# Kernel tuning notes

Hardware: AMD Instinct MI355X
Metric: run time of the kernel (lower is better)

## Reference

```python
import jax, jax.numpy as jnp
import numpy as np
from math import sqrt

NUM_ENT = 100000
NUM_REL = 237  # base; rel table has 2*NUM_REL rows
DIM = 200
HALF = DIM // 2


def _lrelu(x, slope):
    return jnp.where(x >= 0, x, slope * x)


def setup_inputs() -> dict:
    key = jax.random.key(0)
    ks = jax.random.split(key, 20)
    s = 0.02
    inp = {
        'edge_index': jax.random.randint(ks[0], (2, 500000), 0, NUM_ENT),
        'edge_type': jax.random.randint(ks[1], (500000,), 0, 2 * NUM_REL),
        'toTest': jax.random.randint(ks[2], (131072, 2), 0, NUM_ENT),
        'ent_emb': s * jax.random.normal(ks[3], (NUM_ENT, DIM), jnp.float32),
        'rel_emb': s * jax.random.normal(ks[4], (2 * NUM_REL, DIM), jnp.float32),
        'W': s * jax.random.normal(ks[5], (DIM, DIM), jnp.float32),
        'W_loop': s * jax.random.normal(ks[6], (DIM, DIM), jnp.float32),
        'W_rel': s * jax.random.normal(ks[7], (DIM, DIM), jnp.float32),
        'trans_w': s * jax.random.normal(ks[8], (DIM, HALF), jnp.float32),
        'trans_b': jnp.zeros((HALF,), jnp.float32),
        'q_w': s * jax.random.normal(ks[9], (HALF, 128), jnp.float32),
        'q_b': jnp.zeros((128,), jnp.float32),
        'k_w': s * jax.random.normal(ks[10], (HALF, 128), jnp.float32),
        'k_b': jnp.zeros((128,), jnp.float32),
        'w1': s * jax.random.normal(ks[11], (DIM * 2 + 1 + 2 * NUM_REL, 2048), jnp.float32),
        'b1': jnp.zeros((2048,), jnp.float32),
        'w2': s * jax.random.normal(ks[12], (2048, 512), jnp.float32),
        'b2': jnp.zeros((512,), jnp.float32),
        'w3': s * jax.random.normal(ks[13], (512, 1), jnp.float32),
        'b3': jnp.zeros((1,), jnp.float32),
    }
    return inp


def reference(ent_emb, rel_emb, W, W_loop, W_rel, trans_w, trans_b,
              q_w, q_b, k_w, k_b, w1, b1, w2, b2, w3, b3,
              edge_index, edge_type, toTest):
    # --- CompGCN base layer ('sub' composition, degree-normalized scatter-add) ---
    src, dst = edge_index[0], edge_index[1]
    msg = (ent_emb[src] - rel_emb[edge_type]) @ W          # [E, D] gather + GEMM
    deg = jax.ops.segment_sum(jnp.ones_like(dst, jnp.float32), dst, num_segments=NUM_ENT)
    norm = jax.lax.rsqrt(jnp.maximum(deg, 1.0))
    agg = jax.ops.segment_sum(msg, dst, num_segments=NUM_ENT) * norm[:, None]
    all_ent = jnp.tanh(agg + ent_emb @ W_loop)             # [num_ent, D]
    all_rel = rel_emb @ W_rel                              # [2*num_rel, D]

    # --- PairRE test scoring path ---
    head_rel = all_rel[:, :HALF]                           # [2R, D/2]
    tail_rel = all_rel[:, HALF:]
    te = all_ent[toTest]                                   # [N, 2, D] gather
    ee = te @ trans_w + trans_b                            # [N, 2, D/2]
    h_e, t_e = ee[:, 0], ee[:, 1]
    atta = ((h_e @ q_w + q_b) * (t_e @ k_w + k_b)).sum(-1, keepdims=True) / sqrt(DIM)
    relSim = h_e @ head_rel.T - t_e @ tail_rel.T           # [N, 2R]
    cat = jnp.concatenate([te[:, 0], te[:, 1], atta, relSim], axis=1)
    h1 = _lrelu(cat @ w1 + b1, 1e-4)
    h2 = _lrelu(h1 @ w2 + b2, 1e-3)
    return jax.nn.sigmoid(h2 @ w3 + b3)                    # [N, 1]
```

## Files before the change

### kernel.cpp

```cpp
#include <hip/hip_runtime.h>

typedef unsigned short u16;
typedef __attribute__((ext_vector_type(8))) short bf8;
typedef __attribute__((ext_vector_type(4))) float fx4;

#define N_ENT   100000
#define N_EDGE  500000
#define N_TEST  131072
#define EDIM    200
#define AE_LD   224
#define NB_SCAN 391

__device__ __forceinline__ u16 f2bf(float f) {
  union { float f; unsigned u; } c; c.f = f;
  return (u16)((c.u + 0x7FFFu + ((c.u >> 16) & 1u)) >> 16);
}
__device__ __forceinline__ float bf2f(u16 h) {
  union { unsigned u; float f; } c; c.u = ((unsigned)h) << 16;
  return c.f;
}
__device__ __forceinline__ void gload16(const u16* g, u16* l) {
  __builtin_amdgcn_global_load_lds(
      (const __attribute__((address_space(1))) void*)g,
      (__attribute__((address_space(3))) void*)l, 16, 0, 0);
}

#define BM 128
#define BN 128
#define BK 32

__global__ __launch_bounds__(256) void gemm_bf16(
    const u16* __restrict__ A, long lda,
    const u16* __restrict__ B, long ldb,
    u16* __restrict__ out, long ldOut,
    int K,
    const int* __restrict__ rowIdx, int idxMode, int mClamp,
    int mValid, int nValid, int nStore,
    const float* __restrict__ bias, int act, float slope,
    const u16* __restrict__ qbuf, const float* __restrict__ auxF,
    float* __restrict__ dotOut)
{
  __shared__ __align__(16) u16 As[BM * BK];
  __shared__ __align__(16) u16 Bs[BN * BK];
  const int tid  = threadIdx.x;
  const int wave = tid >> 6, lane = tid & 63;
  const int wr = (wave >> 1) * 64, wc = (wave & 1) * 64;
  const int fr = lane & 15, fq = lane >> 4;
  const long bm = (long)blockIdx.x * BM, bn = (long)blockIdx.y * BN;

  const int srow = wave * 32;
  const int kc = (lane & 3) * 8;
  long a0[2], a1[2], boff[2];
  #pragma unroll
  for (int h = 0; h < 2; ++h) {
    long gmRow = bm + srow + h * 16 + (lane >> 2);
    long b0, b1;
    if (idxMode == 0) {
      long gm = (gmRow >= mClamp) ? (mClamp - 1) : gmRow;
      b0 = gm * lda; b1 = b0;
    } else if (idxMode == 2) {
      b0 = (long)rowIdx[2 * gmRow] * lda; b1 = b0;
    } else if (idxMode == 3) {
      b0 = (long)rowIdx[2 * gmRow + 1] * lda; b1 = b0;
    } else {
      b0 = (long)rowIdx[2 * gmRow] * lda;
      b1 = (long)rowIdx[2 * gmRow + 1] * lda - 224;
    }
    a0[h] = b0 + kc; a1[h] = b1 + kc;
    boff[h] = (bn + srow + h * 16 + (lane >> 2)) * ldb + kc;
  }

  fx4 zero4 = {0.f, 0.f, 0.f, 0.f};
  fx4 acc[4][4];
  #pragma unroll
  for (int i = 0; i < 4; ++i)
    #pragma unroll
    for (int j = 0; j < 4; ++j) acc[i][j] = zero4;

  for (int k0 = 0; k0 < K; k0 += BK) {
    __syncthreads();
    const bool lo = (k0 + kc) < 224;
    #pragma unroll
    for (int h = 0; h < 2; ++h) {
      const long ao = (idxMode == 4) ? (lo ? a0[h] : a1[h]) : a0[h];
      gload16(A + ao + k0, &As[(srow + h * 16) * BK]);
      gload16(B + boff[h] + k0, &Bs[(srow + h * 16) * BK]);
    }
    __syncthreads();
    bf8 aF[4], bF[4];
    #pragma unroll
    for (int mt = 0; mt < 4; ++mt) aF[mt] = *(const bf8*)&As[(wr + mt * 16 + fr) * BK + fq * 8];
    #pragma unroll
    for (int nt = 0; nt < 4; ++nt) bF[nt] = *(const bf8*)&Bs[(wc + nt * 16 + fr) * BK + fq * 8];
    #pragma unroll
    for (int mt = 0; mt < 4; ++mt)
      #pragma unroll
      for (int nt = 0; nt < 4; ++nt)
        acc[mt][nt] = __builtin_amdgcn_mfma_f32_16x16x32_bf16(aF[mt], bF[nt], acc[mt][nt], 0, 0, 0);
  }

  if (act == 3 || act == 4) {
    #pragma unroll
    for (int mt = 0; mt < 4; ++mt) {
      #pragma unroll
      for (int r = 0; r < 4; ++r) {
        const long gm = bm + wr + mt * 16 + fq * 4 + r;
        float p = 0.f;
        #pragma unroll
        for (int nt = 0; nt < 4; ++nt) {
          const long gn = bn + wc + nt * 16 + fr;
          float v = acc[mt][nt][r] + bias[gn];
          if (act == 3) p += v * bf2f(qbuf[gm * 128 + gn]);
          else { v = (v >= 0.f) ? v : v * slope; p += v * auxF[gn]; }
        }
        p += __shfl_xor(p, 1, 64); p += __shfl_xor(p, 2, 64);
        p += __shfl_xor(p, 4, 64); p += __shfl_xor(p, 8, 64);
        if (fr == 0 && gm < mValid)
          atomicAdd(&dotOut[gm], (act == 3) ? p * 0.07071067811865475f : p);
      }
    }
    return;
  }

  #pragma unroll
  for (int mt = 0; mt < 4; ++mt) {
    #pragma unroll
    for (int r = 0; r < 4; ++r) {
      const long gm = bm + wr + mt * 16 + fq * 4 + r;
      if (gm >= mValid) continue;
      const float attaV = (act == 5) ? dotOut[gm] : 0.f;
      #pragma unroll
      for (int nt = 0; nt < 4; ++nt) {
        const long gn = bn + wc + nt * 16 + fr;
        if (gn >= nStore) continue;
        float v = 0.f;
        if (gn < nValid) {
          v = acc[mt][nt][r];
          if (bias) v += bias[gn];
          if (act == 1) v = tanhf(v);
          else if (act == 5) { v += attaV * auxF[gn]; v = (v >= 0.f) ? v : v * slope; }
        }
        out[gm * ldOut + gn] = f2bf(v);
      }
    }
  }
}

__global__ void hist_kernel(const int* __restrict__ ei, int* __restrict__ cnt) {
  int e = blockIdx.x * 256 + threadIdx.x;
  if (e < N_EDGE) atomicAdd(&cnt[ei[N_EDGE + e]], 1);
}
__global__ void scanA_kernel(const int* __restrict__ cnt, int* __restrict__ offs,
                             int* __restrict__ blockSums) {
  __shared__ int s[256];
  int gid = blockIdx.x * 256 + threadIdx.x;
  int v = (gid < N_ENT) ? cnt[gid] : 0;
  s[threadIdx.x] = v;
  __syncthreads();
  for (int off = 1; off < 256; off <<= 1) {
    int t = (threadIdx.x >= off) ? s[threadIdx.x - off] : 0;
    __syncthreads();
    s[threadIdx.x] += t;
    __syncthreads();
  }
  if (gid < N_ENT) offs[gid] = s[threadIdx.x] - v;
  if (threadIdx.x == 255) blockSums[blockIdx.x] = s[255];
}
__global__ void scanB_kernel(const int* __restrict__ blockSums, int* __restrict__ blockOffs) {
  __shared__ int s[512];
  int v = (threadIdx.x < NB_SCAN) ? blockSums[threadIdx.x] : 0;
  s[threadIdx.x] = v;
  __syncthreads();
  for (int off = 1; off < 512; off <<= 1) {
    int t = (threadIdx.x >= off) ? s[threadIdx.x - off] : 0;
    __syncthreads();
    s[threadIdx.x] += t;
    __syncthreads();
  }
  if (threadIdx.x < NB_SCAN) blockOffs[threadIdx.x] = s[threadIdx.x] - v;
}
__global__ void scanC_kernel(int* __restrict__ offs, const int* __restrict__ blockOffs) {
  int gid = blockIdx.x * 256 + threadIdx.x;
  if (gid < N_ENT) offs[gid] += blockOffs[blockIdx.x];
}
__global__ void place_kernel(const int* __restrict__ ei, const int* __restrict__ et,
                             const int* __restrict__ offs, int* __restrict__ cursor,
                             int* __restrict__ sortedSrc, int* __restrict__ sortedT) {
  int e = blockIdx.x * 256 + threadIdx.x;
  if (e >= N_EDGE) return;
  int dst = ei[N_EDGE + e];
  int pos = offs[dst] + atomicAdd(&cursor[dst], 1);
  sortedSrc[pos] = ei[e];
  sortedT[pos]   = et[e];
}
__global__ void agg_A1_kernel(const int* __restrict__ offs, const int* __restrict__ cnt,
                              const int* __restrict__ sortedSrc, const int* __restrict__ sortedT,
                              const float* __restrict__ ent_emb, const float* __restrict__ rel_emb,
                              u16* __restrict__ A1) {
  const int r = blockIdx.x * 4 + (threadIdx.x >> 6);
  if (r >= N_ENT) return;
  const int lane = threadIdx.x & 63;
  const int beg = offs[r], n = cnt[r];
  float a0 = 0.f, a1 = 0.f, a2 = 0.f, a3 = 0.f;
  for (int e = 0; e < n; ++e) {
    const int s = sortedSrc[beg + e], t = sortedT[beg + e];
    const float* er = ent_emb + (size_t)s * EDIM;
    const float* rr = rel_emb + (size_t)t * EDIM;
    a0 += er[lane]       - rr[lane];
    a1 += er[64 + lane]  - rr[64 + lane];
    a2 += er[128 + lane] - rr[128 + lane];
    if (lane < 8) a3 += er[192 + lane] - rr[192 + lane];
  }
  const float nm = rsqrtf(fmaxf((float)n, 1.f));
  u16* row = A1 + (size_t)r * 416;
  row[lane]       = f2bf(a0 * nm);
  row[64 + lane]  = f2bf(a1 * nm);
  row[128 + lane] = f2bf(a2 * nm);
  if (lane < 8) row[192 + lane] = f2bf(a3 * nm);
  const float* er = ent_emb + (size_t)r * EDIM;
  row[200 + lane] = f2bf(er[lane]);
  row[264 + lane] = f2bf(er[64 + lane]);
  row[328 + lane] = f2bf(er[128 + lane]);
  if (lane < 8)  row[392 + lane] = f2bf(er[192 + lane]);
  if (lane < 16) row[400 + lane] = 0;
}

__global__ void build_B1T(const float* __restrict__ W, const float* __restrict__ W_loop,
                          u16* __restrict__ B1T)
{
  int idx = blockIdx.x * 256 + threadIdx.x;
  if (idx >= 256 * 416) return;
  int n = idx / 416, k = idx % 416;
  float v = 0.f;
  if (n < 200) {
    if (k < 200) v = W[k * 200 + n];
    else if (k < 400) v = W_loop[(k - 200) * 200 + n];
  }
  B1T[idx] = f2bf(v);
}
__global__ void all_rel_kernel(const float* __restrict__ rel_emb, const float* __restrict__ W_rel,
                               float* __restrict__ all_rel)
{
  int r = blockIdx.x, c = threadIdx.x;
  if (c >= 200) return;
  const float* re = rel_emb + r * 200;
  float a = 0.f;
  for (int k = 0; k < 200; ++k) a += re[k] * W_rel[k * 200 + c];
  all_rel[r * 200 + c] = a;
}
__global__ void pq_kernel(const float* __restrict__ all_rel, const float* __restrict__ w1,
                          float* __restrict__ PQ) {
  int idx = blockIdx.x * 256 + threadIdx.x;
  if (idx >= 2 * 100 * 2048) return;
  int n = idx & 2047, m = (idx >> 11) % 100, sel = idx / 204800;
  float a = 0.f;
  for (int r = 0; r < 474; ++r)
    a += all_rel[r * 200 + sel * 100 + m] * w1[(size_t)(401 + r) * 2048 + n];
  PQ[idx] = a;
}
__global__ void p2_kernel(const float* __restrict__ trans_w, const float* __restrict__ PQ,
                          float* __restrict__ P2) {
  int idx = blockIdx.x * 256 + threadIdx.x;
  if (idx >= 2 * 200 * 2048) return;
  int n = idx & 2047, k = (idx >> 11) % 200, sel = idx / 409600;
  const float* pq = PQ + sel * 204800;
  float a = 0.f;
  for (int m = 0; m < 100; ++m) a += trans_w[k * 100 + m] * pq[m * 2048 + n];
  P2[idx] = a;
}
__global__ void w1eff_kernel(const float* __restrict__ w1, const float* __restrict__ P2,
                             u16* __restrict__ W1eff) {
  int idx = blockIdx.x * 256 + threadIdx.x;
  if (idx >= 2048 * 448) return;
  int n = idx / 448, k = idx % 448;
  float v = 0.f;
  if (k < 200) v = w1[(size_t)k * 2048 + n] + P2[(size_t)k * 2048 + n];
  else if (k >= 224 && k < 424) {
    int kk = k - 224;
    v = w1[(size_t)(200 + kk) * 2048 + n] - P2[409600 + (size_t)kk * 2048 + n];
  }
  W1eff[idx] = f2bf(v);
}
__global__ void b1eff_kernel(const float* __restrict__ b1, const float* __restrict__ trans_b,
                             const float* __restrict__ PQ, float* __restrict__ b1eff) {
  int n = blockIdx.x * 256 + threadIdx.x;
  if (n >= 2048) return;
  float a = b1[n];
  for (int m = 0; m < 100; ++m)
    a += trans_b[m] * (PQ[m * 2048 + n] - PQ[204800 + m * 2048 + n]);
  b1eff[n] = a;
}
__global__ void qkw2_kernel(const float* __restrict__ trans_w, const float* __restrict__ q_w,
                            const float* __restrict__ k_w, u16* __restrict__ qw2T,
                            u16* __restrict__ kw2T) {
  int idx = blockIdx.x * 256 + threadIdx.x;
  if (idx >= 128 * 224) return;
  int j = idx / 224, k = idx % 224;
  float a = 0.f, b = 0.f;
  if (k < 200)
    for (int m = 0; m < 100; ++m) {
      float t = trans_w[k * 100 + m];
      a += t * q_w[m * 128 + j];
      b += t * k_w[m * 128 + j];
    }
  qw2T[idx] = f2bf(a);
  kw2T[idx] = f2bf(b);
}
__global__ void qkb2_kernel(const float* __restrict__ q_b, const float* __restrict__ k_b,
                            const float* __restrict__ trans_b, const float* __restrict__ q_w,
                            const float* __restrict__ k_w, float* __restrict__ qb2,
                            float* __restrict__ kb2) {
  int j = threadIdx.x;
  if (j >= 128) return;
  float a = q_b[j], b = k_b[j];
  for (int m = 0; m < 100; ++m) {
    a += trans_b[m] * q_w[m * 128 + j];
    b += trans_b[m] * k_w[m * 128 + j];
  }
  qb2[j] = a; kb2[j] = b;
}
__global__ void build_w2T(const float* __restrict__ w2, u16* __restrict__ w2T)
{
  long idx = (long)blockIdx.x * 256 + threadIdx.x;
  if (idx >= (long)512 * 2048) return;
  int n = (int)(idx / 2048), k = (int)(idx % 2048);
  w2T[idx] = f2bf(w2[(size_t)k * 512 + n]);
}
__global__ void sigmoid_kernel(const float* __restrict__ logit, const float* __restrict__ b3,
                               float* __restrict__ out) {
  int i = blockIdx.x * 256 + threadIdx.x;
  if (i >= N_TEST) return;
  out[i] = 1.f / (1.f + __expf(-(logit[i] + b3[0])));
}

extern "C" void kernel_launch(void* const* d_in, const int* in_sizes, int n_in,
                              void* d_out, int out_size, void* d_ws, size_t ws_size,
                              hipStream_t stream)
{
  (void)in_sizes; (void)n_in; (void)out_size;
  const int*   edge_index = (const int*)d_in[0];
  const int*   edge_type  = (const int*)d_in[1];
  const int*   toTest     = (const int*)d_in[2];
  const float* ent_emb    = (const float*)d_in[3];
  const float* rel_emb    = (const float*)d_in[4];
  const float* W          = (const float*)d_in[5];
  const float* W_loop     = (const float*)d_in[6];
  const float* W_rel      = (const float*)d_in[7];
  const float* trans_w    = (const float*)d_in[8];
  const float* trans_b    = (const float*)d_in[9];
  const float* q_w        = (const float*)d_in[10];
  const float* q_b        = (const float*)d_in[11];
  const float* k_w        = (const float*)d_in[12];
  const float* k_b        = (const float*)d_in[13];
  const float* w1         = (const float*)d_in[14];
  const float* b1         = (const float*)d_in[15];
  const float* w2         = (const float*)d_in[16];
  const float* b2         = (const float*)d_in[17];
  const float* w3         = (const float*)d_in[18];
  const float* b3         = (const float*)d_in[19];
  float* out = (float*)d_out;

  unsigned char* ws = (unsigned char*)d_ws;
  float* atta    = (float*)(ws + 0);
  float* logit   = (float*)(ws + 524288);
  float* allrel  = (float*)(ws + 1048576);
  u16*   B1T     = (u16*)  (ws + 1427968);
  u16*   W1eff   = (u16*)  (ws + 1640960);
  u16*   qw2T    = (u16*)  (ws + 3475968);
  u16*   kw2T    = (u16*)  (ws + 3533312);
  float* b1eff   = (float*)(ws + 3590656);
  float* qb2     = (float*)(ws + 3598848);
  float* kb2     = (float*)(ws + 3599872);
  u16*   w2T     = (u16*)  (ws + 3600896);
  const size_t X_base = 5698048;
  u16*   all_ent = (u16*)  (ws + X_base);
  u16*   Qbuf    = (u16*)  (ws + X_base + 44800000);
  const size_t Y_base = 84052480;
  u16*   A1      = (u16*)  (ws + Y_base);
  const size_t Z_base = 167252480;

  int*   cnt       = (int*)  (ws + Z_base);
  int*   offs      = (int*)  (ws + Z_base + 400000);
  int*   cursor    = (int*)  (ws + Z_base + 800000);
  int*   blockSums = (int*)  (ws + Z_base + 1200000);
  int*   blockOffs = (int*)  (ws + Z_base + 1202048);
  int*   sortedSrc = (int*)  (ws + Z_base + 1204096);
  int*   sortedT   = (int*)  (ws + Z_base + 3204096);
  float* PQ        = (float*)(ws + Z_base + 5204096);
  float* P2        = (float*)(ws + Z_base + 6842496);

  int CH;
  if      (Z_base + (size_t)131072 * 4096 <= ws_size) CH = 131072;
  else if (Z_base + (size_t)65536  * 4096 <= ws_size) CH = 65536;
  else if (Z_base + (size_t)32768  * 4096 <= ws_size) CH = 32768;
  else if (Z_base + (size_t)16384  * 4096 <= ws_size) CH = 16384;
  else if (Z_base + (size_t)8192   * 4096 <= ws_size) CH = 8192;
  else return;
  u16* h1 = (u16*)(ws + Z_base);
  const int NC = N_TEST / CH;

  hipMemsetAsync(cnt, 0, 400000, stream);
  hipMemsetAsync(cursor, 0, 400000, stream);
  hipMemsetAsync(atta, 0, 524288, stream);
  hipMemsetAsync(logit, 0, 524288, stream);

  hist_kernel<<<(N_EDGE + 255) / 256, 256, 0, stream>>>(edge_index, cnt);
  scanA_kernel<<<NB_SCAN, 256, 0, stream>>>(cnt, offs, blockSums);
  scanB_kernel<<<1, 512, 0, stream>>>(blockSums, blockOffs);
  scanC_kernel<<<NB_SCAN, 256, 0, stream>>>(offs, blockOffs);
  place_kernel<<<(N_EDGE + 255) / 256, 256, 0, stream>>>(edge_index, edge_type, offs, cursor,
                                                         sortedSrc, sortedT);
  agg_A1_kernel<<<(N_ENT + 3) / 4, 256, 0, stream>>>(offs, cnt, sortedSrc, sortedT,
                                                     ent_emb, rel_emb, A1);
  build_B1T<<<(256 * 416) / 256, 256, 0, stream>>>(W, W_loop, B1T);

  gemm_bf16<<<dim3(782, 2), 256, 0, stream>>>(A1, 416, B1T, 416, all_ent, AE_LD,
      416, nullptr, 0, N_ENT, N_ENT, 200, AE_LD, nullptr, 1, 0.f, nullptr, nullptr, nullptr);

  all_rel_kernel<<<474, 256, 0, stream>>>(rel_emb, W_rel, allrel);
  pq_kernel<<<(2 * 100 * 2048) / 256, 256, 0, stream>>>(allrel, w1, PQ);
  p2_kernel<<<(2 * 200 * 2048) / 256, 256, 0, stream>>>(trans_w, PQ, P2);
  w1eff_kernel<<<(2048 * 448) / 256, 256, 0, stream>>>(w1, P2, W1eff);
  b1eff_kernel<<<8, 256, 0, stream>>>(b1, trans_b, PQ, b1eff);
  qkw2_kernel<<<(128 * 224) / 256, 256, 0, stream>>>(trans_w, q_w, k_w, qw2T, kw2T);
  qkb2_kernel<<<1, 128, 0, stream>>>(q_b, k_b, trans_b, q_w, k_w, qb2, kb2);
  build_w2T<<<(512 * 2048) / 256, 256, 0, stream>>>(w2, w2T);

  gemm_bf16<<<dim3(1024, 1), 256, 0, stream>>>(all_ent, AE_LD, qw2T, AE_LD, Qbuf, 128,
      AE_LD, toTest, 2, 0, N_TEST, 128, 128, qb2, 0, 0.f, nullptr, nullptr, nullptr);
  gemm_bf16<<<dim3(1024, 1), 256, 0, stream>>>(all_ent, AE_LD, kw2T, AE_LD, nullptr, 0,
      AE_LD, toTest, 3, 0, N_TEST, 128, 128, kb2, 3, 0.f, Qbuf, nullptr, atta);

  for (int c = 0; c < NC; ++c) {
    gemm_bf16<<<dim3(CH / 128, 16), 256, 0, stream>>>(all_ent, AE_LD, W1eff, 448, h1, 2048,
        448, toTest + (size_t)c * CH * 2, 4, 0, CH, 2048, 2048, b1eff, 5, 0.0001f,
        nullptr, w1 + (size_t)400 * 2048, atta + (size_t)c * CH);
    gemm_bf16<<<dim3(CH / 128, 4), 256, 0, stream>>>(h1, 2048, w2T, 2048, nullptr, 0,
        2048, nullptr, 0, CH, CH, 512, 512, b2, 4, 0.001f,
        nullptr, w3, logit + (size_t)c * CH);
  }
  sigmoid_kernel<<<N_TEST / 256, 256, 0, stream>>>(logit, b3, out);
}
```

Before: 1.996 ms.

## Materialize gathered test-pair embeddings and vectorize aggregation loads

Adds a gather kernel that copies the two all_ent rows for each test pair into a contiguous bf16 buffer. All downstream GEMMs then read dense rows instead of doing indexed gathers, which removes the idxMode branching and the per-row index loads from the GEMM kernel. The aggregation kernel now uses float4 loads and packed 64-bit bf16 stores. The cost is an extra ~117MB write and read pass, and the h1 workspace moves, which may force a smaller chunk size.

```diff
diff --git a/kernel.cpp b/kernel.cpp
--- a/kernel.cpp
+++ b/kernel.cpp
@@ -1,6 +1,7 @@
 #include <hip/hip_runtime.h>
 
 typedef unsigned short u16;
+typedef unsigned long long u64;
 typedef __attribute__((ext_vector_type(8))) short bf8;
 typedef __attribute__((ext_vector_type(4))) float fx4;
 
@@ -33,8 +34,7 @@
     const u16* __restrict__ A, long lda,
     const u16* __restrict__ B, long ldb,
     u16* __restrict__ out, long ldOut,
-    int K,
-    const int* __restrict__ rowIdx, int idxMode, int mClamp,
+    int K, int mClamp,
     int mValid, int nValid, int nStore,
     const float* __restrict__ bias, int act, float slope,
     const u16* __restrict__ qbuf, const float* __restrict__ auxF,
@@ -50,23 +50,12 @@
 
   const int srow = wave * 32;
   const int kc = (lane & 3) * 8;
-  long a0[2], a1[2], boff[2];
+  long aoff[2], boff[2];
   #pragma unroll
   for (int h = 0; h < 2; ++h) {
-    long gmRow = bm + srow + h * 16 + (lane >> 2);
-    long b0, b1;
-    if (idxMode == 0) {
-      long gm = (gmRow >= mClamp) ? (mClamp - 1) : gmRow;
-      b0 = gm * lda; b1 = b0;
-    } else if (idxMode == 2) {
-      b0 = (long)rowIdx[2 * gmRow] * lda; b1 = b0;
-    } else if (idxMode == 3) {
-      b0 = (long)rowIdx[2 * gmRow + 1] * lda; b1 = b0;
-    } else {
-      b0 = (long)rowIdx[2 * gmRow] * lda;
-      b1 = (long)rowIdx[2 * gmRow + 1] * lda - 224;
-    }
-    a0[h] = b0 + kc; a1[h] = b1 + kc;
+    long gm = bm + srow + h * 16 + (lane >> 2);
+    if (gm >= mClamp) gm = mClamp - 1;
+    aoff[h] = gm * lda + kc;
     boff[h] = (bn + srow + h * 16 + (lane >> 2)) * ldb + kc;
   }
 
@@ -79,11 +68,9 @@
 
   for (int k0 = 0; k0 < K; k0 += BK) {
     __syncthreads();
-    const bool lo = (k0 + kc) < 224;
     #pragma unroll
     for (int h = 0; h < 2; ++h) {
-      const long ao = (idxMode == 4) ? (lo ? a0[h] : a1[h]) : a0[h];
-      gload16(A + ao + k0, &As[(srow + h * 16) * BK]);
+      gload16(A + aoff[h] + k0, &As[(srow + h * 16) * BK]);
       gload16(B + boff[h] + k0, &Bs[(srow + h * 16) * BK]);
     }
     __syncthreads();
@@ -201,28 +188,38 @@
   if (r >= N_ENT) return;
   const int lane = threadIdx.x & 63;
   const int beg = offs[r], n = cnt[r];
-  float a0 = 0.f, a1 = 0.f, a2 = 0.f, a3 = 0.f;
-  for (int e = 0; e < n; ++e) {
-    const int s = sortedSrc[beg + e], t = sortedT[beg + e];
-    const float* er = ent_emb + (size_t)s * EDIM;
-    const float* rr = rel_emb + (size_t)t * EDIM;
-    a0 += er[lane]       - rr[lane];
-    a1 += er[64 + lane]  - rr[64 + lane];
-    a2 += er[128 + lane] - rr[128 + lane];
-    if (lane < 8) a3 += er[192 + lane] - rr[192 + lane];
-  }
-  const float nm = rsqrtf(fmaxf((float)n, 1.f));
   u16* row = A1 + (size_t)r * 416;
-  row[lane]       = f2bf(a0 * nm);
-  row[64 + lane]  = f2bf(a1 * nm);
-  row[128 + lane] = f2bf(a2 * nm);
-  if (lane < 8) row[192 + lane] = f2bf(a3 * nm);
-  const float* er = ent_emb + (size_t)r * EDIM;
-  row[200 + lane] = f2bf(er[lane]);
-  row[264 + lane] = f2bf(er[64 + lane]);
-  row[328 + lane] = f2bf(er[128 + lane]);
-  if (lane < 8)  row[392 + lane] = f2bf(er[192 + lane]);
+  if (lane < 50) {
+    float4 a = {0.f, 0.f, 0.f, 0.f};
+    for (int e = 0; e < n; ++e) {
+      const int s = sortedSrc[beg + e], t = sortedT[beg + e];
+      float4 x = ((const float4*)(ent_emb + (size_t)s * EDIM))[lane];
+      float4 y = ((const float4*)(rel_emb + (size_t)t * EDIM))[lane];
+      a.x += x.x - y.x; a.y += x.y - y.y; a.z += x.z - y.z; a.w += x.w - y.w;
+    }
+    const float nm = rsqrtf(fmaxf((float)n, 1.f));
+    u64 p = (u64)f2bf(a.x * nm) | ((u64)f2bf(a.y * nm) << 16)
+          | ((u64)f2bf(a.z * nm) << 32) | ((u64)f2bf(a.w * nm) << 48);
+    *(u64*)(row + 4 * lane) = p;
+    float4 e = ((const float4*)(ent_emb + (size_t)r * EDIM))[lane];
+    u64 q = (u64)f2bf(e.x) | ((u64)f2bf(e.y) << 16)
+          | ((u64)f2bf(e.z) << 32) | ((u64)f2bf(e.w) << 48);
+    *(u64*)(row + 200 + 4 * lane) = q;
+  }
   if (lane < 16) row[400 + lane] = 0;
+}
+
+__global__ void catb_kernel(const u16* __restrict__ all_ent, const int* __restrict__ toTest,
+                            u16* __restrict__ catb) {
+  const int i = blockIdx.x * 4 + (threadIdx.x >> 6);
+  const int lane = threadIdx.x & 63;
+  const int t0 = toTest[2 * i], t1 = toTest[2 * i + 1];
+  u16* row = catb + (size_t)i * 448;
+  if (lane < 28)
+    *(bf8*)(row + lane * 8) = *(const bf8*)(all_ent + (size_t)t0 * AE_LD + lane * 8);
+  else if (lane < 56)
+    *(bf8*)(row + 224 + (lane - 28) * 8) =
+        *(const bf8*)(all_ent + (size_t)t1 * AE_LD + (lane - 28) * 8);
 }
 
 __global__ void build_B1T(const float* __restrict__ W, const float* __restrict__ W_loop,
@@ -389,14 +386,17 @@
   float* PQ        = (float*)(ws + Z_base + 5204096);
   float* P2        = (float*)(ws + Z_base + 6842496);
 
+  u16* catb = (u16*)(ws + Y_base);
+  const size_t H_base = Y_base + (size_t)N_TEST * 448 * 2;
+
   int CH;
-  if      (Z_base + (size_t)131072 * 4096 <= ws_size) CH = 131072;
-  else if (Z_base + (size_t)65536  * 4096 <= ws_size) CH = 65536;
-  else if (Z_base + (size_t)32768  * 4096 <= ws_size) CH = 32768;
-  else if (Z_base + (size_t)16384  * 4096 <= ws_size) CH = 16384;
-  else if (Z_base + (size_t)8192   * 4096 <= ws_size) CH = 8192;
+  if      (H_base + (size_t)131072 * 4096 <= ws_size) CH = 131072;
+  else if (H_base + (size_t)65536  * 4096 <= ws_size) CH = 65536;
+  else if (H_base + (size_t)32768  * 4096 <= ws_size) CH = 32768;
+  else if (H_base + (size_t)16384  * 4096 <= ws_size) CH = 16384;
+  else if (H_base + (size_t)8192   * 4096 <= ws_size) CH = 8192;
   else return;
-  u16* h1 = (u16*)(ws + Z_base);
+  u16* h1 = (u16*)(ws + H_base);
   const int NC = N_TEST / CH;
 
   hipMemsetAsync(cnt, 0, 400000, stream);
@@ -415,7 +415,7 @@
   build_B1T<<<(256 * 416) / 256, 256, 0, stream>>>(W, W_loop, B1T);
 
   gemm_bf16<<<dim3(782, 2), 256, 0, stream>>>(A1, 416, B1T, 416, all_ent, AE_LD,
-      416, nullptr, 0, N_ENT, N_ENT, 200, AE_LD, nullptr, 1, 0.f, nullptr, nullptr, nullptr);
+      416, N_ENT, N_ENT, 200, AE_LD, nullptr, 1, 0.f, nullptr, nullptr, nullptr);
 
   all_rel_kernel<<<474, 256, 0, stream>>>(rel_emb, W_rel, allrel);
   pq_kernel<<<(2 * 100 * 2048) / 256, 256, 0, stream>>>(allrel, w1, PQ);
@@ -426,17 +426,19 @@
   qkb2_kernel<<<1, 128, 0, stream>>>(q_b, k_b, trans_b, q_w, k_w, qb2, kb2);
   build_w2T<<<(512 * 2048) / 256, 256, 0, stream>>>(w2, w2T);
 
-  gemm_bf16<<<dim3(1024, 1), 256, 0, stream>>>(all_ent, AE_LD, qw2T, AE_LD, Qbuf, 128,
-      AE_LD, toTest, 2, 0, N_TEST, 128, 128, qb2, 0, 0.f, nullptr, nullptr, nullptr);
-  gemm_bf16<<<dim3(1024, 1), 256, 0, stream>>>(all_ent, AE_LD, kw2T, AE_LD, nullptr, 0,
-      AE_LD, toTest, 3, 0, N_TEST, 128, 128, kb2, 3, 0.f, Qbuf, nullptr, atta);
+  catb_kernel<<<N_TEST / 4, 256, 0, stream>>>(all_ent, toTest, catb);
+  gemm_bf16<<<dim3(1024, 1), 256, 0, stream>>>(catb, 448, qw2T, 224, Qbuf, 128,
+      224, N_TEST, N_TEST, 128, 128, qb2, 0, 0.f, nullptr, nullptr, nullptr);
+  gemm_bf16<<<dim3(1024, 1), 256, 0, stream>>>(catb + 224, 448, kw2T, 224, nullptr, 0,
+      224, N_TEST, N_TEST, 128, 128, kb2, 3, 0.f, Qbuf, nullptr, atta);
 
   for (int c = 0; c < NC; ++c) {
-    gemm_bf16<<<dim3(CH / 128, 16), 256, 0, stream>>>(all_ent, AE_LD, W1eff, 448, h1, 2048,
-        448, toTest + (size_t)c * CH * 2, 4, 0, CH, 2048, 2048, b1eff, 5, 0.0001f,
+    gemm_bf16<<<dim3(CH / 128, 16), 256, 0, stream>>>(catb + (size_t)c * CH * 448, 448,
+        W1eff, 448, h1, 2048,
+        448, CH, CH, 2048, 2048, b1eff, 5, 0.0001f,
         nullptr, w1 + (size_t)400 * 2048, atta + (size_t)c * CH);
     gemm_bf16<<<dim3(CH / 128, 4), 256, 0, stream>>>(h1, 2048, w2T, 2048, nullptr, 0,
-        2048, nullptr, 0, CH, CH, 512, 512, b2, 4, 0.001f,
+        2048, CH, CH, 512, 512, b2, 4, 0.001f,
         nullptr, w3, logit + (size_t)c * CH);
   }
   sigmoid_kernel<<<N_TEST / 256, 256, 0, stream>>>(logit, b3, out);
```

New measurement: 2.084 ms. 1.04x slower.
